# Kernel optimization log

Measured on AMD Instinct MI355X. Metric: run time of the kernel, lower is better.

The kernel has to match this reference:

```python
import jax, jax.numpy as jnp
import numpy as np

WS = 9       # window_size
GAMMA = 2.0
REAL = False


def box_avg(x, ws):
    """Depthwise uniform box filter with circular padding, weight = 1/ws^2."""
    p = ws // 2
    xp = jnp.pad(x, ((0, 0), (0, 0), (p, p), (p, p)), mode='wrap')  # circular pad
    c = x.shape[1]
    k = jnp.full((c, 1, ws, ws), 1.0 / (ws * ws), dtype=x.dtype)
    return jax.lax.conv_general_dilated(
        xp, k, window_strides=(1, 1), padding='VALID',
        dimension_numbers=('NCHW', 'OIHW', 'NCHW'), feature_group_count=c)


def local_variance(x, ws):
    # E[x^2] - (E[x])^2 per channel over the circular box window
    return box_avg(x * x, ws) - jnp.square(box_avg(x, ws))


def setup_inputs() -> dict:
    key = jax.random.key(0)
    x = jax.random.normal(key, (16, 3, 512, 512), dtype=jnp.float32)
    return {"x": x}


def reference(x):
    # alpha_map: mean over channels of per-channel local variance of x
    alpha_map = local_variance(x, WS).sum(1, keepdims=True) / 3
    # beta_map: local variance of the channel-mean image
    beta_map = local_variance(x.sum(1, keepdims=True) / 3, WS)
    # weight map from variance of x - x with channels reversed ([2,1,0])
    weight = local_variance(x - x[:, ::-1], WS).sum(1, keepdims=True) / 3
    _, _, w, h = weight.shape
    w_sum = weight.sum()
    weight = jnp.exp(-GAMMA * w * h * weight / w_sum)
    w_sum = weight.sum()
    scale = 9.0 / 4.0 if REAL else 3.0 / 2.0
    return scale * (weight * (alpha_map - beta_map)).sum() / w_sum
```

## Files before the change

### kernel.cpp

```cpp
#include <hip/hip_runtime.h>
#include <math.h>

#define N_ 16
#define H_ 512
#define W_ 512
#define HW_ (H_ * W_)
#define BAND 8
#define GAMMA_ 2.0f

__device__ __forceinline__ float wave_reduce(float v) {
#pragma unroll
    for (int off = 32; off > 0; off >>= 1)
        v += __shfl_down(v, off, 64);
    return v;
}

__global__ __launch_bounds__(256) void passA(const float* __restrict__ x,
                                             float* __restrict__ scalars) {
    __shared__ float rowbuf[3][W_];
    __shared__ float red[4];

    const int tid = threadIdx.x;
    const int c0 = tid * 2;
    const int y0 = blockIdx.x * BAND;
    const int b = blockIdx.y;
    const float* xb = x + (size_t)b * (3 * HW_);
    const float inv81 = 1.0f / 81.0f;

    float va[3][2];
#pragma unroll
    for (int f = 0; f < 3; ++f) va[f][0] = va[f][1] = 0.0f;

    auto rowlite = [&](int r, float sgn) {
        int rr = r & (H_ - 1);
        const float* p = xb + rr * W_ + c0;
        float2 a0 = *(const float2*)(p);
        float2 a2 = *(const float2*)(p + 2 * HW_);
#pragma unroll
        for (int i = 0; i < 2; ++i) {
            float x0 = i ? a0.y : a0.x;
            float x2 = i ? a2.y : a2.x;
            float d = x0 - x2;
            va[0][i] = fmaf(sgn, x0, va[0][i]);
            va[1][i] = fmaf(sgn, x2, va[1][i]);
            va[2][i] = fmaf(sgn, d * d, va[2][i]);
        }
    };

#pragma unroll
    for (int k = 0; k < 9; ++k) rowlite(y0 - 4 + k, 1.0f);

    float accwr = 0.0f;
    for (int y = y0; y < y0 + BAND; ++y) {
#pragma unroll
        for (int f = 0; f < 3; ++f)
            *(float2*)&rowbuf[f][c0] = make_float2(va[f][0], va[f][1]);
        __syncthreads();

        float hs[3][2];
#pragma unroll
        for (int f = 0; f < 3; ++f) {
            float2 v[5];
#pragma unroll
            for (int j = 0; j < 5; ++j)
                v[j] = *(const float2*)&rowbuf[f][(c0 + 2 * j - 4) & (W_ - 1)];
            float s0 = ((v[0].x + v[0].y) + (v[1].x + v[1].y)) +
                       ((v[2].x + v[2].y) + (v[3].x + v[3].y)) + v[4].x;
            hs[f][0] = s0;
            hs[f][1] = s0 - v[0].x + v[4].y;
        }
#pragma unroll
        for (int i = 0; i < 2; ++i) {
            float md = (hs[0][i] - hs[1][i]) * inv81;
            accwr += (2.0f / 3.0f) * (hs[2][i] * inv81 - md * md);
        }
        __syncthreads();

        if (y + 1 < y0 + BAND) {
            rowlite(y + 5, 1.0f);
            rowlite(y - 4, -1.0f);
        }
    }

    float s = wave_reduce(accwr);
    if ((tid & 63) == 0) red[tid >> 6] = s;
    __syncthreads();
    if (tid == 0) atomicAdd(&scalars[0], (red[0] + red[1]) + (red[2] + red[3]));
}

__global__ __launch_bounds__(256) void passB(const float* __restrict__ x,
                                             float* __restrict__ scalars) {
    __shared__ float rowbuf[6][W_];
    __shared__ float red[8];

    const int tid = threadIdx.x;
    const int c0 = tid * 2;
    const int y0 = blockIdx.x * BAND;
    const int b = blockIdx.y;
    const float* xb = x + (size_t)b * (3 * HW_);
    const float inv81 = 1.0f / 81.0f;
    const float coef = GAMMA_ * (float)HW_ / scalars[0];

    float vs[6][2];
#pragma unroll
    for (int f = 0; f < 6; ++f) vs[f][0] = vs[f][1] = 0.0f;

    auto row_update = [&](int r, float sgn) {
        int rr = r & (H_ - 1);
        const float* p = xb + rr * W_ + c0;
        float2 a0 = *(const float2*)(p);
        float2 a1 = *(const float2*)(p + HW_);
        float2 a2 = *(const float2*)(p + 2 * HW_);
#pragma unroll
        for (int i = 0; i < 2; ++i) {
            float x0 = i ? a0.y : a0.x;
            float x1 = i ? a1.y : a1.x;
            float x2 = i ? a2.y : a2.x;
            float yv = (x0 + x1 + x2) * (1.0f / 3.0f);
            float d = x0 - x2;
            vs[0][i] = fmaf(sgn, x0, vs[0][i]);
            vs[1][i] = fmaf(sgn, x1, vs[1][i]);
            vs[2][i] = fmaf(sgn, x2, vs[2][i]);
            vs[3][i] = fmaf(sgn, x0 * x0 + x1 * x1 + x2 * x2, vs[3][i]);
            vs[4][i] = fmaf(sgn, yv * yv, vs[4][i]);
            vs[5][i] = fmaf(sgn, d * d, vs[5][i]);
        }
    };

#pragma unroll
    for (int k = 0; k < 9; ++k) row_update(y0 - 4 + k, 1.0f);

    float accw = 0.0f, accwd = 0.0f;

    for (int y = y0; y < y0 + BAND; ++y) {
#pragma unroll
        for (int f = 0; f < 6; ++f)
            *(float2*)&rowbuf[f][c0] = make_float2(vs[f][0], vs[f][1]);
        __syncthreads();

        float hs[6][2];
#pragma unroll
        for (int f = 0; f < 6; ++f) {
            float2 v[5];
#pragma unroll
            for (int j = 0; j < 5; ++j)
                v[j] = *(const float2*)&rowbuf[f][(c0 + 2 * j - 4) & (W_ - 1)];
            float s0 = ((v[0].x + v[0].y) + (v[1].x + v[1].y)) +
                       ((v[2].x + v[2].y) + (v[3].x + v[3].y)) + v[4].x;
            hs[f][0] = s0;
            hs[f][1] = s0 - v[0].x + v[4].y;
        }

#pragma unroll
        for (int i = 0; i < 2; ++i) {
            float B0 = hs[0][i] * inv81, B1 = hs[1][i] * inv81, B2 = hs[2][i] * inv81;
            float alpha = (hs[3][i] * inv81 - (B0 * B0 + B1 * B1 + B2 * B2)) * (1.0f / 3.0f);
            float my = (B0 + B1 + B2) * (1.0f / 3.0f);
            float beta = hs[4][i] * inv81 - my * my;
            float md = B0 - B2;
            float wr = (2.0f / 3.0f) * (hs[5][i] * inv81 - md * md);
            float df = alpha - beta;
            float w = __expf(-coef * wr);
            accw += w;
            accwd += w * df;
        }
        __syncthreads();

        if (y + 1 < y0 + BAND) {
            row_update(y + 5, 1.0f);
            row_update(y - 4, -1.0f);
        }
    }

    float s0 = wave_reduce(accw);
    float s1 = wave_reduce(accwd);
    if ((tid & 63) == 0) {
        red[tid >> 6] = s0;
        red[4 + (tid >> 6)] = s1;
    }
    __syncthreads();
    if (tid == 0) {
        atomicAdd(&scalars[1], (red[0] + red[1]) + (red[2] + red[3]));
        atomicAdd(&scalars[2], (red[4] + red[5]) + (red[6] + red[7]));
    }
}

__global__ void final_kernel(const float* __restrict__ scalars, float* __restrict__ out) {
    out[0] = 1.5f * scalars[2] / scalars[1];
}

extern "C" void kernel_launch(void* const* d_in, const int* in_sizes, int n_in,
                              void* d_out, int out_size, void* d_ws, size_t ws_size,
                              hipStream_t stream) {
    const float* x = (const float*)d_in[0];
    float* out = (float*)d_out;
    float* scalars = (float*)d_ws;

    hipMemsetAsync(d_ws, 0, 16, stream);

    dim3 grid(H_ / BAND, N_);
    passA<<<grid, 256, 0, stream>>>(x, scalars);
    passB<<<grid, 256, 0, stream>>>(x, scalars);
    final_kernel<<<1, 1, 0, stream>>>(scalars, out);
}
```

Measured before the change: 139.2 us.

## Double-buffer row sums in LDS, prefetch next rows, halve band height

Both passes now keep two shared-memory row buffers, alternated each iteration, which removes the second __syncthreads per row. The global loads for the entering and leaving rows are issued before the barrier so their latency can overlap the horizontal-sum work. BAND drops from 8 to 4, doubling the grid for more parallelism. In exchange the 9-row vertical warm-up is paid twice as often relative to useful rows, and LDS use per block doubles.

```diff
diff --git a/kernel.cpp b/kernel.cpp
--- a/kernel.cpp
+++ b/kernel.cpp
@@ -5,7 +5,7 @@
 #define H_ 512
 #define W_ 512
 #define HW_ (H_ * W_)
-#define BAND 8
+#define BAND 4
 #define GAMMA_ 2.0f
 
 __device__ __forceinline__ float wave_reduce(float v) {
@@ -17,7 +17,7 @@
 
 __global__ __launch_bounds__(256) void passA(const float* __restrict__ x,
                                              float* __restrict__ scalars) {
-    __shared__ float rowbuf[3][W_];
+    __shared__ float rowbuf[2][3][W_];
     __shared__ float red[4];
 
     const int tid = threadIdx.x;
@@ -31,11 +31,7 @@
 #pragma unroll
     for (int f = 0; f < 3; ++f) va[f][0] = va[f][1] = 0.0f;
 
-    auto rowlite = [&](int r, float sgn) {
-        int rr = r & (H_ - 1);
-        const float* p = xb + rr * W_ + c0;
-        float2 a0 = *(const float2*)(p);
-        float2 a2 = *(const float2*)(p + 2 * HW_);
+    auto apply = [&](float2 a0, float2 a2, float sgn) {
 #pragma unroll
         for (int i = 0; i < 2; ++i) {
             float x0 = i ? a0.y : a0.x;
@@ -48,13 +44,29 @@
     };
 
 #pragma unroll
-    for (int k = 0; k < 9; ++k) rowlite(y0 - 4 + k, 1.0f);
+    for (int k = 0; k < 9; ++k) {
+        int rr = (y0 - 4 + k) & (H_ - 1);
+        const float* p = xb + rr * W_ + c0;
+        apply(*(const float2*)(p), *(const float2*)(p + 2 * HW_), 1.0f);
+    }
 
     float accwr = 0.0f;
-    for (int y = y0; y < y0 + BAND; ++y) {
+    float2 na0, na2, pa0, pa2;
+
+    for (int it = 0; it < BAND; ++it) {
+        const int y = y0 + it;
+        const int slot = it & 1;
 #pragma unroll
         for (int f = 0; f < 3; ++f)
-            *(float2*)&rowbuf[f][c0] = make_float2(va[f][0], va[f][1]);
+            *(float2*)&rowbuf[slot][f][c0] = make_float2(va[f][0], va[f][1]);
+
+        const bool more = (it + 1 < BAND);
+        if (more) {
+            const float* pa = xb + ((y + 5) & (H_ - 1)) * W_ + c0;
+            const float* ps = xb + ((y - 4) & (H_ - 1)) * W_ + c0;
+            na0 = *(const float2*)(pa); na2 = *(const float2*)(pa + 2 * HW_);
+            pa0 = *(const float2*)(ps); pa2 = *(const float2*)(ps + 2 * HW_);
+        }
         __syncthreads();
 
         float hs[3][2];
@@ -63,7 +75,7 @@
             float2 v[5];
 #pragma unroll
             for (int j = 0; j < 5; ++j)
-                v[j] = *(const float2*)&rowbuf[f][(c0 + 2 * j - 4) & (W_ - 1)];
+                v[j] = *(const float2*)&rowbuf[slot][f][(c0 + 2 * j - 4) & (W_ - 1)];
             float s0 = ((v[0].x + v[0].y) + (v[1].x + v[1].y)) +
                        ((v[2].x + v[2].y) + (v[3].x + v[3].y)) + v[4].x;
             hs[f][0] = s0;
@@ -74,11 +86,10 @@
             float md = (hs[0][i] - hs[1][i]) * inv81;
             accwr += (2.0f / 3.0f) * (hs[2][i] * inv81 - md * md);
         }
-        __syncthreads();
-
-        if (y + 1 < y0 + BAND) {
-            rowlite(y + 5, 1.0f);
-            rowlite(y - 4, -1.0f);
+
+        if (more) {
+            apply(na0, na2, 1.0f);
+            apply(pa0, pa2, -1.0f);
         }
     }
 
@@ -90,7 +101,7 @@
 
 __global__ __launch_bounds__(256) void passB(const float* __restrict__ x,
                                              float* __restrict__ scalars) {
-    __shared__ float rowbuf[6][W_];
+    __shared__ float rowbuf[2][6][W_];
     __shared__ float red[8];
 
     const int tid = threadIdx.x;
@@ -105,12 +116,7 @@
 #pragma unroll
     for (int f = 0; f < 6; ++f) vs[f][0] = vs[f][1] = 0.0f;
 
-    auto row_update = [&](int r, float sgn) {
-        int rr = r & (H_ - 1);
-        const float* p = xb + rr * W_ + c0;
-        float2 a0 = *(const float2*)(p);
-        float2 a1 = *(const float2*)(p + HW_);
-        float2 a2 = *(const float2*)(p + 2 * HW_);
+    auto apply = [&](float2 a0, float2 a1, float2 a2, float sgn) {
 #pragma unroll
         for (int i = 0; i < 2; ++i) {
             float x0 = i ? a0.y : a0.x;
@@ -128,14 +134,33 @@
     };
 
 #pragma unroll
-    for (int k = 0; k < 9; ++k) row_update(y0 - 4 + k, 1.0f);
+    for (int k = 0; k < 9; ++k) {
+        int rr = (y0 - 4 + k) & (H_ - 1);
+        const float* p = xb + rr * W_ + c0;
+        apply(*(const float2*)(p), *(const float2*)(p + HW_), *(const float2*)(p + 2 * HW_), 1.0f);
+    }
 
     float accw = 0.0f, accwd = 0.0f;
-
-    for (int y = y0; y < y0 + BAND; ++y) {
+    float2 na0, na1, na2, pa0, pa1, pa2;
+
+    for (int it = 0; it < BAND; ++it) {
+        const int y = y0 + it;
+        const int slot = it & 1;
 #pragma unroll
         for (int f = 0; f < 6; ++f)
-            *(float2*)&rowbuf[f][c0] = make_float2(vs[f][0], vs[f][1]);
+            *(float2*)&rowbuf[slot][f][c0] = make_float2(vs[f][0], vs[f][1]);
+
+        const bool more = (it + 1 < BAND);
+        if (more) {
+            const float* pa = xb + ((y + 5) & (H_ - 1)) * W_ + c0;
+            const float* ps = xb + ((y - 4) & (H_ - 1)) * W_ + c0;
+            na0 = *(const float2*)(pa);
+            na1 = *(const float2*)(pa + HW_);
+            na2 = *(const float2*)(pa + 2 * HW_);
+            pa0 = *(const float2*)(ps);
+            pa1 = *(const float2*)(ps + HW_);
+            pa2 = *(const float2*)(ps + 2 * HW_);
+        }
         __syncthreads();
 
         float hs[6][2];
@@ -144,7 +169,7 @@
             float2 v[5];
 #pragma unroll
             for (int j = 0; j < 5; ++j)
-                v[j] = *(const float2*)&rowbuf[f][(c0 + 2 * j - 4) & (W_ - 1)];
+                v[j] = *(const float2*)&rowbuf[slot][f][(c0 + 2 * j - 4) & (W_ - 1)];
             float s0 = ((v[0].x + v[0].y) + (v[1].x + v[1].y)) +
                        ((v[2].x + v[2].y) + (v[3].x + v[3].y)) + v[4].x;
             hs[f][0] = s0;
@@ -164,11 +189,10 @@
             accw += w;
             accwd += w * df;
         }
-        __syncthreads();
-
-        if (y + 1 < y0 + BAND) {
-            row_update(y + 5, 1.0f);
-            row_update(y - 4, -1.0f);
+
+        if (more) {
+            apply(na0, na1, na2, 1.0f);
+            apply(pa0, pa1, pa2, -1.0f);
         }
     }
 
```

Measured after the change: 168.9 us. +21.3%, slower.
